# Kernel optimization log

Measured on AMD Instinct MI355X. Metric: run time of the kernel, lower is better.

## Reference

```python
import jax, jax.numpy as jnp
import numpy as np

INPUT_DIM = 32
HIDDEN = 64
BATCH = 4096
SEQ = 256


def _uniform(key, shape, bound):
    return jax.random.uniform(key, shape, dtype=jnp.float32, minval=-bound, maxval=bound)


def setup_inputs() -> dict:
    key = jax.random.key(0)
    ks = jax.random.split(key, 16)
    kb = 1.0 / np.sqrt(HIDDEN)  # torch LSTM/Linear init bound
    x = jax.random.normal(ks[0], (BATCH, SEQ, INPUT_DIM), dtype=jnp.float32)
    # LSTM layer 0 (input_dim -> hidden), gate order i,f,g,o stacked on dim 0
    Wih0 = _uniform(ks[1], (4 * HIDDEN, INPUT_DIM), kb)
    Whh0 = _uniform(ks[2], (4 * HIDDEN, HIDDEN), kb)
    bih0 = _uniform(ks[3], (4 * HIDDEN,), kb)
    bhh0 = _uniform(ks[4], (4 * HIDDEN,), kb)
    # LSTM layer 1 (hidden -> hidden)
    Wih1 = _uniform(ks[5], (4 * HIDDEN, HIDDEN), kb)
    Whh1 = _uniform(ks[6], (4 * HIDDEN, HIDDEN), kb)
    bih1 = _uniform(ks[7], (4 * HIDDEN,), kb)
    bhh1 = _uniform(ks[8], (4 * HIDDEN,), kb)
    # MLP head
    W1 = _uniform(ks[9], (HIDDEN, HIDDEN), kb)
    b1 = _uniform(ks[10], (HIDDEN,), kb)
    W2 = _uniform(ks[11], (1, HIDDEN), kb)
    b2 = _uniform(ks[12], (1,), kb)
    return {"x": x, "Wih0": Wih0, "Whh0": Whh0, "bih0": bih0, "bhh0": bhh0,
            "Wih1": Wih1, "Whh1": Whh1, "bih1": bih1, "bhh1": bhh1,
            "W1": W1, "b1": b1, "W2": W2, "b2": b2}


def lstm_layer(x, Wih, Whh, bih, bhh):
    """x: [B,T,D] -> hidden sequence [B,T,H]. PyTorch gate order i,f,g,o."""
    B = x.shape[0]
    H = Whh.shape[1]
    # precompute input contribution for all timesteps: [B,T,4H]
    gx = jnp.einsum('btd,gd->btg', x, Wih) + bih + bhh

    def step(carry, g_t):
        h, c = carry
        g = g_t + h @ Whh.T  # [B,4H]
        i, f, gg, o = jnp.split(g, 4, axis=-1)
        i = jax.nn.sigmoid(i)
        f = jax.nn.sigmoid(f)
        gg = jnp.tanh(gg)
        o = jax.nn.sigmoid(o)
        c = f * c + i * gg
        h = o * jnp.tanh(c)
        return (h, c), h

    h0 = jnp.zeros((B, H), x.dtype)
    c0 = jnp.zeros((B, H), x.dtype)
    _, hs = jax.lax.scan(step, (h0, c0), jnp.swapaxes(gx, 0, 1))  # hs: [T,B,H]
    return jnp.swapaxes(hs, 0, 1)


def reference(x, Wih0, Whh0, bih0, bhh0, Wih1, Whh1, bih1, bhh1, W1, b1, W2, b2):
    h1 = lstm_layer(x, Wih0, Whh0, bih0, bhh0)    # [B,T,H]
    h2 = lstm_layer(h1, Wih1, Whh1, bih1, bhh1)   # [B,T,H]
    last = h2[:, -1, :]                            # [B,H]
    f = jax.nn.relu(last @ W1.T + b1)              # dropout = identity (eval)
    out = f @ W2.T + b2                            # [B,1]
    return out
```

## Files before the change

### kernel.cpp

```cpp
#include <hip/hip_runtime.h>
#include <cstdint>

typedef __attribute__((ext_vector_type(8))) _Float16 f16x8;
typedef __attribute__((ext_vector_type(4))) float f32x4;

#define SEQL 256

#define WS_B0H   0
#define WS_B0L   49152
#define WS_B1H   98304
#define WS_BIAS0 229376
#define WS_BIAS1 230400

#define ASTR 656
#define L_A  0
#define L_HD 10496
#define HDSTR 272
#define LDS_TOTAL 14848

#define NEG_L   -1.4426950408889634f
#define NEG_2L  -2.8853900817779268f
#define LO_SCALE 2048.0f
#define LO_INV   4.8828125e-4f

__device__ __forceinline__ float ex2(float x) { return __builtin_amdgcn_exp2f(x); }
__device__ __forceinline__ float rcp_(float x) { return __builtin_amdgcn_rcpf(x); }
__device__ __forceinline__ f32x4 mfma16(f16x8 a, f16x8 b, f32x4 c) {
  return __builtin_amdgcn_mfma_f32_16x16x32_f16(a, b, c, 0, 0, 0);
}
__device__ __forceinline__ f16x8 zero8() {
  f16x8 z;
#pragma unroll
  for (int i = 0; i < 8; ++i) z[i] = (_Float16)0.f;
  return z;
}

__global__ __launch_bounds__(256) void prep(
    const float* __restrict__ Wih0, const float* __restrict__ Whh0,
    const float* __restrict__ bih0, const float* __restrict__ bhh0,
    const float* __restrict__ Wih1, const float* __restrict__ Whh1,
    const float* __restrict__ bih1, const float* __restrict__ bhh1,
    unsigned char* __restrict__ ws) {
  int e = blockIdx.x * 256 + threadIdx.x;
  if (e < 24576) {
    int j = e & 7, lane = (e >> 3) & 63, nt = (e >> 9) & 15, ks = e >> 13;
    int kdim = ks * 32 + (lane >> 4) * 8 + j;
    int col = nt * 16 + (lane & 15);
    int ko = col >> 2, g = col & 3;
    float w = (kdim < 32) ? Wih0[(g * 64 + ko) * 32 + kdim]
                          : Whh0[(g * 64 + ko) * 64 + (kdim - 32)];
    w *= (g == 2) ? NEG_2L : NEG_L;
    _Float16 hi = (_Float16)w;
    _Float16 lo = (_Float16)((w - (float)hi) * LO_SCALE);
    ((_Float16*)(ws + WS_B0H))[e] = hi;
    ((_Float16*)(ws + WS_B0L))[e] = lo;
  } else if (e < 57344) {
    int r = e - 24576;
    int j = r & 7, lane = (r >> 3) & 63, nt = (r >> 9) & 15, ks = r >> 13;
    int kdim = ks * 32 + (lane >> 4) * 8 + j;
    int col = nt * 16 + (lane & 15);
    int ko = col >> 2, g = col & 3;
    float w = (kdim < 64) ? Wih1[(g * 64 + ko) * 64 + kdim]
                          : Whh1[(g * 64 + ko) * 64 + (kdim - 64)];
    w *= (g == 2) ? NEG_2L : NEG_L;
    _Float16 hi = (_Float16)w;
    _Float16 lo = (_Float16)((w - (float)hi) * LO_SCALE);
    ((_Float16*)(ws + WS_B1H))[r] = hi;
    ((_Float16*)(ws + WS_B1H + 65536))[r] = lo;
  } else if (e < 57856) {
    int r = e - 57344;
    int col = r & 255, ko = col >> 2, g = col & 3;
    float v = (r < 256) ? bih0[g * 64 + ko] + bhh0[g * 64 + ko]
                        : bih1[g * 64 + ko] + bhh1[g * 64 + ko];
    v *= (g == 2) ? NEG_2L : NEG_L;
    ((float*)(ws + (r < 256 ? WS_BIAS0 : WS_BIAS1)))[col] = v;
  }
}

__global__ __launch_bounds__(1024, 4) void lstm_mfma6(
    const float* __restrict__ x, const unsigned char* __restrict__ ws,
    const float* __restrict__ W1, const float* __restrict__ b1,
    const float* __restrict__ W2, const float* __restrict__ b2,
    float* __restrict__ out) {
  __shared__ __align__(16) unsigned char lds[LDS_TOTAL];
  const int tid = threadIdx.x;
  const int lane = tid & 63, wave = tid >> 6;
  const int q = lane >> 4, bcol = lane & 15;

  f16x8 b0h[3], b0l[3], b1h[4], b1l[4];
#pragma unroll
  for (int ks = 0; ks < 3; ++ks) {
    int rec = (ks * 16 + wave) * 64 + lane;
    b0h[ks] = ((const f16x8*)(ws + WS_B0H))[rec];
    b0l[ks] = ((const f16x8*)(ws + WS_B0L))[rec];
  }
#pragma unroll
  for (int ks = 0; ks < 4; ++ks) {
    int rec = (ks * 16 + wave) * 64 + lane;
    b1h[ks] = ((const f16x8*)(ws + WS_B1H))[rec];
    b1l[ks] = ((const f16x8*)(ws + WS_B1H + 65536))[rec];
  }
  const f32x4 bias0v = ((const f32x4*)(ws + WS_BIAS0))[wave * 4 + q];
  const f32x4 bias1v = ((const f32x4*)(ws + WS_BIAS1))[wave * 4 + q];
  f32x4 z4;
  z4[0] = z4[1] = z4[2] = z4[3] = 0.f;

  for (int i = tid; i < 2624; i += 1024) ((unsigned*)(lds + L_A))[i] = 0u;

  const bool do_x = tid < 512;
  const int bx = tid >> 5, d = tid & 31;
  const float* xcol = x + (size_t)(blockIdx.x * 16 + (do_x ? bx : 0)) * (SEQL * 32) + d;
  if (do_x) {
    *(_Float16*)(lds + L_A + bx * ASTR + d * 2) = (_Float16)xcol[0];
  }

  const int ard = bcol * ASTR + q * 16;
  const int hwr = bcol * ASTR + (wave * 4 + q) * 2;

  float c1 = 0.f, c2 = 0.f, h2f = 0.f;
  f16x8 ah1[2], ah2[2], ax;
  ah1[0] = ah1[1] = ah2[0] = ah2[1] = zero8();
  __syncthreads();
  ax = *(const f16x8*)(lds + L_A + ard + 0);

  auto cell = [&](const f32x4& aH, const f32x4& aL, float& c) -> float {
    float p0 = fmaf(aL[0], LO_INV, aH[0]);
    float p1 = fmaf(aL[1], LO_INV, aH[1]);
    float p2 = fmaf(aL[2], LO_INV, aH[2]);
    float p3 = fmaf(aL[3], LO_INV, aH[3]);
    float gi = rcp_(1.f + ex2(p0));
    float gf = rcp_(1.f + ex2(p1));
    float gg = fmaf(2.f, rcp_(1.f + ex2(p2)), -1.f);
    float go = rcp_(1.f + ex2(p3));
    c = fmaf(gf, c, gi * gg);
    float tc = fmaf(2.f, rcp_(1.f + ex2(c * NEG_2L)), -1.f);
    return go * tc;
  };

  auto iter = [&](int t, int par, bool doL2) {
    const int h1s = 128 + par * 128;
    const int h2s = 384 + par * 128;
    const int xwr = (par ^ 1) * 64;
    float xnext = 0.f;
    if (do_x && t < SEQL - 1) xnext = xcol[(t + 1) * 32];

    f32x4 aH0 = mfma16(b0h[0], ax, bias0v);
    f32x4 aL0 = mfma16(b0l[0], ax, z4);
    f32x4 aH1 = mfma16(b1h[0], ah1[0], bias1v);
    f32x4 aL1 = mfma16(b1l[0], ah1[0], z4);
    aH1 = mfma16(b1h[1], ah1[1], aH1);
    aL1 = mfma16(b1l[1], ah1[1], aL1);
#pragma unroll
    for (int ks = 0; ks < 2; ++ks) {
      aH0 = mfma16(b0h[ks + 1], ah1[ks], aH0);
      aL0 = mfma16(b0l[ks + 1], ah1[ks], aL0);
      aH1 = mfma16(b1h[ks + 2], ah2[ks], aH1);
      aL1 = mfma16(b1l[ks + 2], ah2[ks], aL1);
    }
    float h1 = cell(aH0, aL0, c1);
    *(_Float16*)(lds + L_A + hwr + h1s) = (_Float16)h1;
    if (doL2) {
      float h2 = cell(aH1, aL1, c2);
      *(_Float16*)(lds + L_A + hwr + h2s) = (_Float16)h2;
    }
    if (do_x && t < SEQL - 1) {
      *(_Float16*)(lds + L_A + bx * ASTR + xwr + d * 2) = (_Float16)xnext;
    }
    __syncthreads();
    ah1[0] = *(const f16x8*)(lds + L_A + ard + h1s);
    ah1[1] = *(const f16x8*)(lds + L_A + ard + h1s + 64);
    ah2[0] = *(const f16x8*)(lds + L_A + ard + h2s);
    ah2[1] = *(const f16x8*)(lds + L_A + ard + h2s + 64);
    ax     = *(const f16x8*)(lds + L_A + ard + xwr);
  };

  iter(0, 0, false);
#pragma unroll 1
  for (int tp = 0; tp < 127; ++tp) {
    iter(2 * tp + 1, 1, true);
    iter(2 * tp + 2, 0, true);
  }
  iter(255, 1, true);

  {
    f32x4 aH = mfma16(b1h[0], ah1[0], bias1v);
    f32x4 aL = mfma16(b1l[0], ah1[0], z4);
    aH = mfma16(b1h[1], ah1[1], aH);
    aL = mfma16(b1l[1], ah1[1], aL);
#pragma unroll
    for (int ks = 0; ks < 2; ++ks) {
      aH = mfma16(b1h[ks + 2], ah2[ks], aH);
      aL = mfma16(b1l[ks + 2], ah2[ks], aL);
    }
    h2f = cell(aH, aL, c2);
  }

  __syncthreads();
  *(float*)(lds + L_HD + bcol * HDSTR + (wave * 4 + q) * 4) = h2f;
  __syncthreads();
  if (tid < 256) {
    const int s = tid & 15, bo = tid >> 4;
    const float* h2row = (const float*)(lds + L_HD + bo * HDSTR);
    float partial = 0.f;
#pragma unroll
    for (int kk4 = 0; kk4 < 4; ++kk4) {
      int kk = s * 4 + kk4;
      float f = b1[kk];
#pragma unroll
      for (int j = 0; j < 64; j += 4) {
        f32x4 w = *(const f32x4*)(W1 + kk * 64 + j);
        f = fmaf(w[0], h2row[j], f);
        f = fmaf(w[1], h2row[j + 1], f);
        f = fmaf(w[2], h2row[j + 2], f);
        f = fmaf(w[3], h2row[j + 3], f);
      }
      f = fmaxf(f, 0.f);
      partial = fmaf(f, W2[kk], partial);
    }
    partial += __shfl_xor(partial, 8, 64);
    partial += __shfl_xor(partial, 4, 64);
    partial += __shfl_xor(partial, 2, 64);
    partial += __shfl_xor(partial, 1, 64);
    if (s == 0) out[blockIdx.x * 16 + bo] = partial + b2[0];
  }
}

extern "C" void kernel_launch(void* const* d_in, const int* in_sizes, int n_in,
                              void* d_out, int out_size, void* d_ws, size_t ws_size,
                              hipStream_t stream) {
  const float* x    = (const float*)d_in[0];
  const float* Wih0 = (const float*)d_in[1];
  const float* Whh0 = (const float*)d_in[2];
  const float* bih0 = (const float*)d_in[3];
  const float* bhh0 = (const float*)d_in[4];
  const float* Wih1 = (const float*)d_in[5];
  const float* Whh1 = (const float*)d_in[6];
  const float* bih1 = (const float*)d_in[7];
  const float* bhh1 = (const float*)d_in[8];
  const float* W1   = (const float*)d_in[9];
  const float* b1   = (const float*)d_in[10];
  const float* W2   = (const float*)d_in[11];
  const float* b2   = (const float*)d_in[12];
  unsigned char* ws = (unsigned char*)d_ws;
  float* out = (float*)d_out;

  prep<<<(57856 + 255) / 256, 256, 0, stream>>>(Wih0, Whh0, bih0, bhh0,
                                                Wih1, Whh1, bih1, bhh1, ws);
  lstm_mfma6<<<256, 1024, 0, stream>>>(x, ws, W1, b1, W2, b2, out);
}
```

Baseline: 442.9 us.

## Specialize waves per LSTM layer and load x directly into registers

Splits the 16 waves into two groups: 8 waves compute layer 0 and 8 compute layer 1, with each wave owning two column tiles. Before, every wave computed a slice of both layers. The input x is now read straight from global memory into MFMA operand registers with one step of prefetch, replacing the LDS staging path, and the LDS layout shrinks to match. This cuts redundant operand reads and x staging per step, but doubles the MFMA chain length per wave and may leave the two wave groups unevenly loaded.

After: 541.6 us. 1.22x slower.

```diff
diff --git a/kernel.cpp b/kernel.cpp
--- a/kernel.cpp
+++ b/kernel.cpp
@@ -12,11 +12,11 @@
 #define WS_BIAS0 229376
 #define WS_BIAS1 230400
 
-#define ASTR 656
+#define ASTR 528
 #define L_A  0
-#define L_HD 10496
+#define L_HD 8448
 #define HDSTR 272
-#define LDS_TOTAL 14848
+#define LDS_TOTAL 12800
 
 #define NEG_L   -1.4426950408889634f
 #define NEG_2L  -2.8853900817779268f
@@ -28,11 +28,13 @@
 __device__ __forceinline__ f32x4 mfma16(f16x8 a, f16x8 b, f32x4 c) {
   return __builtin_amdgcn_mfma_f32_16x16x32_f16(a, b, c, 0, 0, 0);
 }
-__device__ __forceinline__ f16x8 zero8() {
-  f16x8 z;
-#pragma unroll
-  for (int i = 0; i < 8; ++i) z[i] = (_Float16)0.f;
-  return z;
+__device__ __forceinline__ f16x8 cvt8(f32x4 a, f32x4 b) {
+  f16x8 r;
+#pragma unroll
+  for (int j = 0; j < 4; ++j) r[j] = (_Float16)a[j];
+#pragma unroll
+  for (int j = 0; j < 4; ++j) r[4 + j] = (_Float16)b[j];
+  return r;
 }
 
 __global__ __launch_bounds__(256) void prep(
@@ -77,7 +79,7 @@
   }
 }
 
-__global__ __launch_bounds__(1024, 4) void lstm_mfma6(
+__global__ __launch_bounds__(1024, 4) void lstm_mfma7(
     const float* __restrict__ x, const unsigned char* __restrict__ ws,
     const float* __restrict__ W1, const float* __restrict__ b1,
     const float* __restrict__ W2, const float* __restrict__ b2,
@@ -86,42 +88,49 @@
   const int tid = threadIdx.x;
   const int lane = tid & 63, wave = tid >> 6;
   const int q = lane >> 4, bcol = lane & 15;
-
-  f16x8 b0h[3], b0l[3], b1h[4], b1l[4];
-#pragma unroll
-  for (int ks = 0; ks < 3; ++ks) {
-    int rec = (ks * 16 + wave) * 64 + lane;
-    b0h[ks] = ((const f16x8*)(ws + WS_B0H))[rec];
-    b0l[ks] = ((const f16x8*)(ws + WS_B0L))[rec];
-  }
-#pragma unroll
-  for (int ks = 0; ks < 4; ++ks) {
-    int rec = (ks * 16 + wave) * 64 + lane;
-    b1h[ks] = ((const f16x8*)(ws + WS_B1H))[rec];
-    b1l[ks] = ((const f16x8*)(ws + WS_B1H + 65536))[rec];
-  }
-  const f32x4 bias0v = ((const f32x4*)(ws + WS_BIAS0))[wave * 4 + q];
-  const f32x4 bias1v = ((const f32x4*)(ws + WS_BIAS1))[wave * 4 + q];
+  const int wtype = wave >> 3;
+  const int wn = wave & 7;
+
+  f16x8 wh[2][4], wl[2][4];
+  if (wtype == 0) {
+#pragma unroll
+    for (int m = 0; m < 2; ++m)
+#pragma unroll
+      for (int ks = 0; ks < 3; ++ks) {
+        int rec = (ks * 16 + (wn + 8 * m)) * 64 + lane;
+        wh[m][ks] = ((const f16x8*)(ws + WS_B0H))[rec];
+        wl[m][ks] = ((const f16x8*)(ws + WS_B0L))[rec];
+      }
+  } else {
+#pragma unroll
+    for (int m = 0; m < 2; ++m)
+#pragma unroll
+      for (int ks = 0; ks < 4; ++ks) {
+        int rec = (ks * 16 + (wn + 8 * m)) * 64 + lane;
+        wh[m][ks] = ((const f16x8*)(ws + WS_B1H))[rec];
+        wl[m][ks] = ((const f16x8*)(ws + WS_B1H + 65536))[rec];
+      }
+  }
+  const f32x4* bp = (const f32x4*)(ws + (wtype ? WS_BIAS1 : WS_BIAS0));
+  const f32x4 bias0v = bp[4 * wn + q];
+  const f32x4 bias1v = bp[4 * (wn + 8) + q];
   f32x4 z4;
   z4[0] = z4[1] = z4[2] = z4[3] = 0.f;
 
-  for (int i = tid; i < 2624; i += 1024) ((unsigned*)(lds + L_A))[i] = 0u;
-
-  const bool do_x = tid < 512;
-  const int bx = tid >> 5, d = tid & 31;
-  const float* xcol = x + (size_t)(blockIdx.x * 16 + (do_x ? bx : 0)) * (SEQL * 32) + d;
-  if (do_x) {
-    *(_Float16*)(lds + L_A + bx * ASTR + d * 2) = (_Float16)xcol[0];
-  }
-
-  const int ard = bcol * ASTR + q * 16;
-  const int hwr = bcol * ASTR + (wave * 4 + q) * 2;
-
-  float c1 = 0.f, c2 = 0.f, h2f = 0.f;
-  f16x8 ah1[2], ah2[2], ax;
-  ah1[0] = ah1[1] = ah2[0] = ah2[1] = zero8();
+  for (int i2 = tid; i2 < 2112; i2 += 1024) ((unsigned*)lds)[i2] = 0u;
+
+  const float* xp = x + (size_t)(blockIdx.x * 16 + bcol) * (SEQL * 32) + q * 8;
+  f16x8 ax;
+  f32x4 xna, xnb;
+  if (wtype == 0) {
+    f32x4 a0 = *(const f32x4*)(xp);
+    f32x4 b0v = *(const f32x4*)(xp + 4);
+    ax = cvt8(a0, b0v);
+    xna = *(const f32x4*)(xp + 32);
+    xnb = *(const f32x4*)(xp + 36);
+  }
+  float cc0 = 0.f, cc1 = 0.f;
   __syncthreads();
-  ax = *(const f16x8*)(lds + L_A + ard + 0);
 
   auto cell = [&](const f32x4& aH, const f32x4& aL, float& c) -> float {
     float p0 = fmaf(aL[0], LO_INV, aH[0]);
@@ -137,41 +146,60 @@
     return go * tc;
   };
 
-  auto iter = [&](int t, int par, bool doL2) {
-    const int h1s = 128 + par * 128;
-    const int h2s = 384 + par * 128;
-    const int xwr = (par ^ 1) * 64;
-    float xnext = 0.f;
-    if (do_x && t < SEQL - 1) xnext = xcol[(t + 1) * 32];
-
-    f32x4 aH0 = mfma16(b0h[0], ax, bias0v);
-    f32x4 aL0 = mfma16(b0l[0], ax, z4);
-    f32x4 aH1 = mfma16(b1h[0], ah1[0], bias1v);
-    f32x4 aL1 = mfma16(b1l[0], ah1[0], z4);
-    aH1 = mfma16(b1h[1], ah1[1], aH1);
-    aL1 = mfma16(b1l[1], ah1[1], aL1);
-#pragma unroll
-    for (int ks = 0; ks < 2; ++ks) {
-      aH0 = mfma16(b0h[ks + 1], ah1[ks], aH0);
-      aL0 = mfma16(b0l[ks + 1], ah1[ks], aL0);
-      aH1 = mfma16(b1h[ks + 2], ah2[ks], aH1);
-      aL1 = mfma16(b1l[ks + 2], ah2[ks], aL1);
-    }
-    float h1 = cell(aH0, aL0, c1);
-    *(_Float16*)(lds + L_A + hwr + h1s) = (_Float16)h1;
-    if (doL2) {
-      float h2 = cell(aH1, aL1, c2);
-      *(_Float16*)(lds + L_A + hwr + h2s) = (_Float16)h2;
-    }
-    if (do_x && t < SEQL - 1) {
-      *(_Float16*)(lds + L_A + bx * ASTR + xwr + d * 2) = (_Float16)xnext;
+  auto iter = [&](int i, int par, bool doL2) {
+    const int rb = bcol * ASTR;
+    f16x8 ah1a = *(const f16x8*)(lds + rb + (par ^ 1) * 128 + q * 16);
+    f16x8 ah1b = *(const f16x8*)(lds + rb + (par ^ 1) * 128 + 64 + q * 16);
+    if (wtype == 0) {
+      f32x4 aH0 = mfma16(wh[0][0], ax, bias0v);
+      f32x4 aL0 = mfma16(wl[0][0], ax, z4);
+      f32x4 aH1 = mfma16(wh[1][0], ax, bias1v);
+      f32x4 aL1 = mfma16(wl[1][0], ax, z4);
+      aH0 = mfma16(wh[0][1], ah1a, aH0);
+      aL0 = mfma16(wl[0][1], ah1a, aL0);
+      aH1 = mfma16(wh[1][1], ah1a, aH1);
+      aL1 = mfma16(wl[1][1], ah1a, aL1);
+      aH0 = mfma16(wh[0][2], ah1b, aH0);
+      aL0 = mfma16(wl[0][2], ah1b, aL0);
+      aH1 = mfma16(wh[1][2], ah1b, aH1);
+      aL1 = mfma16(wl[1][2], ah1b, aL1);
+      float h0 = cell(aH0, aL0, cc0);
+      float h1v = cell(aH1, aL1, cc1);
+      const int wb = rb + par * 128;
+      *(_Float16*)(lds + wb + (4 * wn + q) * 2) = (_Float16)h0;
+      *(_Float16*)(lds + wb + (4 * (wn + 8) + q) * 2) = (_Float16)h1v;
+      ax = cvt8(xna, xnb);
+      int tn = i + 2; if (tn > SEQL - 1) tn = SEQL - 1;
+      xna = *(const f32x4*)(xp + tn * 32);
+      xnb = *(const f32x4*)(xp + tn * 32 + 4);
+    } else {
+      f16x8 ah2a = *(const f16x8*)(lds + rb + 256 + par * 128 + q * 16);
+      f16x8 ah2b = *(const f16x8*)(lds + rb + 256 + par * 128 + 64 + q * 16);
+      f32x4 aH0 = mfma16(wh[0][0], ah1a, bias0v);
+      f32x4 aL0 = mfma16(wl[0][0], ah1a, z4);
+      f32x4 aH1 = mfma16(wh[1][0], ah1a, bias1v);
+      f32x4 aL1 = mfma16(wl[1][0], ah1a, z4);
+      aH0 = mfma16(wh[0][1], ah1b, aH0);
+      aL0 = mfma16(wl[0][1], ah1b, aL0);
+      aH1 = mfma16(wh[1][1], ah1b, aH1);
+      aL1 = mfma16(wl[1][1], ah1b, aL1);
+      aH0 = mfma16(wh[0][2], ah2a, aH0);
+      aL0 = mfma16(wl[0][2], ah2a, aL0);
+      aH1 = mfma16(wh[1][2], ah2a, aH1);
+      aL1 = mfma16(wl[1][2], ah2a, aL1);
+      aH0 = mfma16(wh[0][3], ah2b, aH0);
+      aL0 = mfma16(wl[0][3], ah2b, aL0);
+      aH1 = mfma16(wh[1][3], ah2b, aH1);
+      aL1 = mfma16(wl[1][3], ah2b, aL1);
+      if (doL2) {
+        float h0 = cell(aH0, aL0, cc0);
+        float h1v = cell(aH1, aL1, cc1);
+        const int wb = rb + 256 + (par ^ 1) * 128;
+        *(_Float16*)(lds + wb + (4 * wn + q) * 2) = (_Float16)h0;
+        *(_Float16*)(lds + wb + (4 * (wn + 8) + q) * 2) = (_Float16)h1v;
+      }
     }
     __syncthreads();
-    ah1[0] = *(const f16x8*)(lds + L_A + ard + h1s);
-    ah1[1] = *(const f16x8*)(lds + L_A + ard + h1s + 64);
-    ah2[0] = *(const f16x8*)(lds + L_A + ard + h2s);
-    ah2[1] = *(const f16x8*)(lds + L_A + ard + h2s + 64);
-    ax     = *(const f16x8*)(lds + L_A + ard + xwr);
   };
 
   iter(0, 0, false);
@@ -182,22 +210,35 @@
   }
   iter(255, 1, true);
 
-  {
-    f32x4 aH = mfma16(b1h[0], ah1[0], bias1v);
-    f32x4 aL = mfma16(b1l[0], ah1[0], z4);
-    aH = mfma16(b1h[1], ah1[1], aH);
-    aL = mfma16(b1l[1], ah1[1], aL);
-#pragma unroll
-    for (int ks = 0; ks < 2; ++ks) {
-      aH = mfma16(b1h[ks + 2], ah2[ks], aH);
-      aL = mfma16(b1l[ks + 2], ah2[ks], aL);
-    }
-    h2f = cell(aH, aL, c2);
-  }
-
+  if (wtype == 1) {
+    const int rb = bcol * ASTR;
+    f16x8 a1 = *(const f16x8*)(lds + rb + 128 + q * 16);
+    f16x8 a1b = *(const f16x8*)(lds + rb + 128 + 64 + q * 16);
+    f16x8 a2 = *(const f16x8*)(lds + rb + 256 + q * 16);
+    f16x8 a2b = *(const f16x8*)(lds + rb + 256 + 64 + q * 16);
+    f32x4 aH0 = mfma16(wh[0][0], a1, bias0v);
+    f32x4 aL0 = mfma16(wl[0][0], a1, z4);
+    f32x4 aH1 = mfma16(wh[1][0], a1, bias1v);
+    f32x4 aL1 = mfma16(wl[1][0], a1, z4);
+    aH0 = mfma16(wh[0][1], a1b, aH0);
+    aL0 = mfma16(wl[0][1], a1b, aL0);
+    aH1 = mfma16(wh[1][1], a1b, aH1);
+    aL1 = mfma16(wl[1][1], a1b, aL1);
+    aH0 = mfma16(wh[0][2], a2, aH0);
+    aL0 = mfma16(wl[0][2], a2, aL0);
+    aH1 = mfma16(wh[1][2], a2, aH1);
+    aL1 = mfma16(wl[1][2], a2, aL1);
+    aH0 = mfma16(wh[0][3], a2b, aH0);
+    aL0 = mfma16(wl[0][3], a2b, aL0);
+    aH1 = mfma16(wh[1][3], a2b, aH1);
+    aL1 = mfma16(wl[1][3], a2b, aL1);
+    float h2f0 = cell(aH0, aL0, cc0);
+    float h2f1 = cell(aH1, aL1, cc1);
+    *(float*)(lds + L_HD + bcol * HDSTR + (4 * wn + q) * 4) = h2f0;
+    *(float*)(lds + L_HD + bcol * HDSTR + (4 * (wn + 8) + q) * 4) = h2f1;
+  }
   __syncthreads();
-  *(float*)(lds + L_HD + bcol * HDSTR + (wave * 4 + q) * 4) = h2f;
-  __syncthreads();
+
   if (tid < 256) {
     const int s = tid & 15, bo = tid >> 4;
     const float* h2row = (const float*)(lds + L_HD + bo * HDSTR);
@@ -246,5 +287,5 @@
 
   prep<<<(57856 + 255) / 256, 256, 0, stream>>>(Wih0, Whh0, bih0, bhh0,
                                                 Wih1, Whh1, bih1, bhh1, ws);
-  lstm_mfma6<<<256, 1024, 0, stream>>>(x, ws, W1, b1, W2, b2, out);
-}
+  lstm_mfma7<<<256, 1024, 0, stream>>>(x, ws, W1, b1, W2, b2, out);
+}
```

## Halve block to 8 waves, each computing two gate tiles, load x directly to registers

Applied to the files above, without the earlier changes.

The LSTM kernel now uses 512 threads (8 waves) per 16-sequence block instead of 1024, and each wave computes two 16-column gate tiles, doubling its register-held weights and MFMA work per step. The input x is read straight from global memory into the MFMA operand registers two steps ahead, which removes the LDS x staging buffer and shrinks the LDS row stride. The aim is to cut the per-timestep barrier cost and LDS traffic by syncing fewer waves and giving each wave more independent MFMAs to interleave. In exchange, register pressure is higher and each wave carries a longer serial chain of work per step.

Measured after the change: 460.2 us. 1.04x slower.

```diff
diff --git a/kernel.cpp b/kernel.cpp
--- a/kernel.cpp
+++ b/kernel.cpp
@@ -12,11 +12,10 @@
 #define WS_BIAS0 229376
 #define WS_BIAS1 230400
 
-#define ASTR 656
-#define L_A  0
-#define L_HD 10496
+#define ASTR 528
+#define L_HD 8448
 #define HDSTR 272
-#define LDS_TOTAL 14848
+#define LDS_TOTAL 12800
 
 #define NEG_L   -1.4426950408889634f
 #define NEG_2L  -2.8853900817779268f
@@ -33,6 +32,14 @@
 #pragma unroll
   for (int i = 0; i < 8; ++i) z[i] = (_Float16)0.f;
   return z;
+}
+__device__ __forceinline__ f16x8 cvt8(f32x4 a, f32x4 b) {
+  f16x8 r;
+#pragma unroll
+  for (int j = 0; j < 4; ++j) r[j] = (_Float16)a[j];
+#pragma unroll
+  for (int j = 0; j < 4; ++j) r[4 + j] = (_Float16)b[j];
+  return r;
 }
 
 __global__ __launch_bounds__(256) void prep(
@@ -77,7 +84,7 @@
   }
 }
 
-__global__ __launch_bounds__(1024, 4) void lstm_mfma6(
+__global__ __launch_bounds__(512, 2) void lstm_mfma9(
     const float* __restrict__ x, const unsigned char* __restrict__ ws,
     const float* __restrict__ W1, const float* __restrict__ b1,
     const float* __restrict__ W2, const float* __restrict__ b2,
@@ -85,43 +92,51 @@
   __shared__ __align__(16) unsigned char lds[LDS_TOTAL];
   const int tid = threadIdx.x;
   const int lane = tid & 63, wave = tid >> 6;
-  const int q = lane >> 4, bcol = lane & 15;
-
-  f16x8 b0h[3], b0l[3], b1h[4], b1l[4];
-#pragma unroll
-  for (int ks = 0; ks < 3; ++ks) {
-    int rec = (ks * 16 + wave) * 64 + lane;
-    b0h[ks] = ((const f16x8*)(ws + WS_B0H))[rec];
-    b0l[ks] = ((const f16x8*)(ws + WS_B0L))[rec];
-  }
-#pragma unroll
-  for (int ks = 0; ks < 4; ++ks) {
-    int rec = (ks * 16 + wave) * 64 + lane;
-    b1h[ks] = ((const f16x8*)(ws + WS_B1H))[rec];
-    b1l[ks] = ((const f16x8*)(ws + WS_B1H + 65536))[rec];
-  }
-  const f32x4 bias0v = ((const f32x4*)(ws + WS_BIAS0))[wave * 4 + q];
-  const f32x4 bias1v = ((const f32x4*)(ws + WS_BIAS1))[wave * 4 + q];
+  const int q = lane >> 4, mcol = lane & 15;
+
+  f16x8 w0h[2][3], w0l[2][3], w1h[2][4], w1l[2][4];
+#pragma unroll
+  for (int m = 0; m < 2; ++m) {
+    const int nt = wave + 8 * m;
+#pragma unroll
+    for (int ks = 0; ks < 3; ++ks) {
+      int rec = (ks * 16 + nt) * 64 + lane;
+      w0h[m][ks] = ((const f16x8*)(ws + WS_B0H))[rec];
+      w0l[m][ks] = ((const f16x8*)(ws + WS_B0L))[rec];
+    }
+#pragma unroll
+    for (int ks = 0; ks < 4; ++ks) {
+      int rec = (ks * 16 + nt) * 64 + lane;
+      w1h[m][ks] = ((const f16x8*)(ws + WS_B1H))[rec];
+      w1l[m][ks] = ((const f16x8*)(ws + WS_B1H + 65536))[rec];
+    }
+  }
+  f32x4 b0v[2], b1v[2];
+#pragma unroll
+  for (int m = 0; m < 2; ++m) {
+    b0v[m] = ((const f32x4*)(ws + WS_BIAS0))[4 * (wave + 8 * m) + q];
+    b1v[m] = ((const f32x4*)(ws + WS_BIAS1))[4 * (wave + 8 * m) + q];
+  }
   f32x4 z4;
   z4[0] = z4[1] = z4[2] = z4[3] = 0.f;
 
-  for (int i = tid; i < 2624; i += 1024) ((unsigned*)(lds + L_A))[i] = 0u;
-
-  const bool do_x = tid < 512;
-  const int bx = tid >> 5, d = tid & 31;
-  const float* xcol = x + (size_t)(blockIdx.x * 16 + (do_x ? bx : 0)) * (SEQL * 32) + d;
-  if (do_x) {
-    *(_Float16*)(lds + L_A + bx * ASTR + d * 2) = (_Float16)xcol[0];
-  }
-
-  const int ard = bcol * ASTR + q * 16;
-  const int hwr = bcol * ASTR + (wave * 4 + q) * 2;
-
-  float c1 = 0.f, c2 = 0.f, h2f = 0.f;
-  f16x8 ah1[2], ah2[2], ax;
+  for (int i = tid; i < 2112; i += 512) ((unsigned*)lds)[i] = 0u;
+
+  const float* xp = x + (size_t)(blockIdx.x * 16 + mcol) * (SEQL * 32) + q * 8;
+  f32x4 x0a = *(const f32x4*)(xp);
+  f32x4 x0b = *(const f32x4*)(xp + 4);
+  f16x8 ax = cvt8(x0a, x0b);
+  f32x4 xna = *(const f32x4*)(xp + 32);
+  f32x4 xnb = *(const f32x4*)(xp + 36);
+
+  const int ard = mcol * ASTR + q * 16;
+  const int wr0 = mcol * ASTR + (4 * wave + q) * 2;
+  const int wr1 = mcol * ASTR + (4 * wave + 32 + q) * 2;
+
+  float c1[2] = {0.f, 0.f}, c2[2] = {0.f, 0.f};
+  f16x8 ah1[2], ah2[2];
   ah1[0] = ah1[1] = ah2[0] = ah2[1] = zero8();
   __syncthreads();
-  ax = *(const f16x8*)(lds + L_A + ard + 0);
 
   auto cell = [&](const f32x4& aH, const f32x4& aL, float& c) -> float {
     float p0 = fmaf(aL[0], LO_INV, aH[0]);
@@ -138,40 +153,56 @@
   };
 
   auto iter = [&](int t, int par, bool doL2) {
-    const int h1s = 128 + par * 128;
-    const int h2s = 384 + par * 128;
-    const int xwr = (par ^ 1) * 64;
-    float xnext = 0.f;
-    if (do_x && t < SEQL - 1) xnext = xcol[(t + 1) * 32];
-
-    f32x4 aH0 = mfma16(b0h[0], ax, bias0v);
-    f32x4 aL0 = mfma16(b0l[0], ax, z4);
-    f32x4 aH1 = mfma16(b1h[0], ah1[0], bias1v);
-    f32x4 aL1 = mfma16(b1l[0], ah1[0], z4);
-    aH1 = mfma16(b1h[1], ah1[1], aH1);
-    aL1 = mfma16(b1l[1], ah1[1], aL1);
-#pragma unroll
-    for (int ks = 0; ks < 2; ++ks) {
-      aH0 = mfma16(b0h[ks + 1], ah1[ks], aH0);
-      aL0 = mfma16(b0l[ks + 1], ah1[ks], aL0);
-      aH1 = mfma16(b1h[ks + 2], ah2[ks], aH1);
-      aL1 = mfma16(b1l[ks + 2], ah2[ks], aL1);
-    }
-    float h1 = cell(aH0, aL0, c1);
-    *(_Float16*)(lds + L_A + hwr + h1s) = (_Float16)h1;
+    const int h1s = par * 128;
+    const int h2s = 256 + par * 128;
+    f32x4 aH0[2], aL0[2], aH1[2], aL1[2];
+    aH0[0] = mfma16(w0h[0][0], ax, b0v[0]);
+    aH0[1] = mfma16(w0h[1][0], ax, b0v[1]);
+    aL0[0] = mfma16(w0l[0][0], ax, z4);
+    aL0[1] = mfma16(w0l[1][0], ax, z4);
+    aH1[0] = mfma16(w1h[0][0], ah1[0], b1v[0]);
+    aH1[1] = mfma16(w1h[1][0], ah1[0], b1v[1]);
+    aL1[0] = mfma16(w1l[0][0], ah1[0], z4);
+    aL1[1] = mfma16(w1l[1][0], ah1[0], z4);
+    aH0[0] = mfma16(w0h[0][1], ah1[0], aH0[0]);
+    aH0[1] = mfma16(w0h[1][1], ah1[0], aH0[1]);
+    aL0[0] = mfma16(w0l[0][1], ah1[0], aL0[0]);
+    aL0[1] = mfma16(w0l[1][1], ah1[0], aL0[1]);
+    aH0[0] = mfma16(w0h[0][2], ah1[1], aH0[0]);
+    aH0[1] = mfma16(w0h[1][2], ah1[1], aH0[1]);
+    aL0[0] = mfma16(w0l[0][2], ah1[1], aL0[0]);
+    aL0[1] = mfma16(w0l[1][2], ah1[1], aL0[1]);
+    aH1[0] = mfma16(w1h[0][1], ah1[1], aH1[0]);
+    aH1[1] = mfma16(w1h[1][1], ah1[1], aH1[1]);
+    aL1[0] = mfma16(w1l[0][1], ah1[1], aL1[0]);
+    aL1[1] = mfma16(w1l[1][1], ah1[1], aL1[1]);
+    aH1[0] = mfma16(w1h[0][2], ah2[0], aH1[0]);
+    aH1[1] = mfma16(w1h[1][2], ah2[0], aH1[1]);
+    aL1[0] = mfma16(w1l[0][2], ah2[0], aL1[0]);
+    aL1[1] = mfma16(w1l[1][2], ah2[0], aL1[1]);
+    aH1[0] = mfma16(w1h[0][3], ah2[1], aH1[0]);
+    aH1[1] = mfma16(w1h[1][3], ah2[1], aH1[1]);
+    aL1[0] = mfma16(w1l[0][3], ah2[1], aL1[0]);
+    aL1[1] = mfma16(w1l[1][3], ah2[1], aL1[1]);
+    float h10 = cell(aH0[0], aL0[0], c1[0]);
+    float h11 = cell(aH0[1], aL0[1], c1[1]);
+    *(_Float16*)(lds + wr0 + h1s) = (_Float16)h10;
+    *(_Float16*)(lds + wr1 + h1s) = (_Float16)h11;
     if (doL2) {
-      float h2 = cell(aH1, aL1, c2);
-      *(_Float16*)(lds + L_A + hwr + h2s) = (_Float16)h2;
-    }
-    if (do_x && t < SEQL - 1) {
-      *(_Float16*)(lds + L_A + bx * ASTR + xwr + d * 2) = (_Float16)xnext;
-    }
+      float h20 = cell(aH1[0], aL1[0], c2[0]);
+      float h21 = cell(aH1[1], aL1[1], c2[1]);
+      *(_Float16*)(lds + wr0 + h2s) = (_Float16)h20;
+      *(_Float16*)(lds + wr1 + h2s) = (_Float16)h21;
+    }
+    ax = cvt8(xna, xnb);
+    int tn = t + 2; if (tn > SEQL - 1) tn = SEQL - 1;
+    xna = *(const f32x4*)(xp + tn * 32);
+    xnb = *(const f32x4*)(xp + tn * 32 + 4);
     __syncthreads();
-    ah1[0] = *(const f16x8*)(lds + L_A + ard + h1s);
-    ah1[1] = *(const f16x8*)(lds + L_A + ard + h1s + 64);
-    ah2[0] = *(const f16x8*)(lds + L_A + ard + h2s);
-    ah2[1] = *(const f16x8*)(lds + L_A + ard + h2s + 64);
-    ax     = *(const f16x8*)(lds + L_A + ard + xwr);
+    ah1[0] = *(const f16x8*)(lds + ard + h1s);
+    ah1[1] = *(const f16x8*)(lds + ard + h1s + 64);
+    ah2[0] = *(const f16x8*)(lds + ard + h2s);
+    ah2[1] = *(const f16x8*)(lds + ard + h2s + 64);
   };
 
   iter(0, 0, false);
@@ -183,21 +214,30 @@
   iter(255, 1, true);
 
   {
-    f32x4 aH = mfma16(b1h[0], ah1[0], bias1v);
-    f32x4 aL = mfma16(b1l[0], ah1[0], z4);
-    aH = mfma16(b1h[1], ah1[1], aH);
-    aL = mfma16(b1l[1], ah1[1], aL);
-#pragma unroll
-    for (int ks = 0; ks < 2; ++ks) {
-      aH = mfma16(b1h[ks + 2], ah2[ks], aH);
-      aL = mfma16(b1l[ks + 2], ah2[ks], aL);
-    }
-    h2f = cell(aH, aL, c2);
-  }
-
+    f32x4 aH[2], aL[2];
+    aH[0] = mfma16(w1h[0][0], ah1[0], b1v[0]);
+    aH[1] = mfma16(w1h[1][0], ah1[0], b1v[1]);
+    aL[0] = mfma16(w1l[0][0], ah1[0], z4);
+    aL[1] = mfma16(w1l[1][0], ah1[0], z4);
+    aH[0] = mfma16(w1h[0][1], ah1[1], aH[0]);
+    aH[1] = mfma16(w1h[1][1], ah1[1], aH[1]);
+    aL[0] = mfma16(w1l[0][1], ah1[1], aL[0]);
+    aL[1] = mfma16(w1l[1][1], ah1[1], aL[1]);
+    aH[0] = mfma16(w1h[0][2], ah2[0], aH[0]);
+    aH[1] = mfma16(w1h[1][2], ah2[0], aH[1]);
+    aL[0] = mfma16(w1l[0][2], ah2[0], aL[0]);
+    aL[1] = mfma16(w1l[1][2], ah2[0], aL[1]);
+    aH[0] = mfma16(w1h[0][3], ah2[1], aH[0]);
+    aH[1] = mfma16(w1h[1][3], ah2[1], aH[1]);
+    aL[0] = mfma16(w1l[0][3], ah2[1], aL[0]);
+    aL[1] = mfma16(w1l[1][3], ah2[1], aL[1]);
+    float h20 = cell(aH[0], aL[0], c2[0]);
+    float h21 = cell(aH[1], aL[1], c2[1]);
+    *(float*)(lds + L_HD + mcol * HDSTR + (4 * wave + q) * 4) = h20;
+    *(float*)(lds + L_HD + mcol * HDSTR + (4 * wave + 32 + q) * 4) = h21;
+  }
   __syncthreads();
-  *(float*)(lds + L_HD + bcol * HDSTR + (wave * 4 + q) * 4) = h2f;
-  __syncthreads();
+
   if (tid < 256) {
     const int s = tid & 15, bo = tid >> 4;
     const float* h2row = (const float*)(lds + L_HD + bo * HDSTR);
@@ -246,5 +286,5 @@
 
   prep<<<(57856 + 255) / 256, 256, 0, stream>>>(Wih0, Whh0, bih0, bhh0,
                                                 Wih1, Whh1, bih1, bhh1, ws);
-  lstm_mfma6<<<256, 1024, 0, stream>>>(x, ws, W1, b1, W2, b2, out);
-}
+  lstm_mfma9<<<256, 512, 0, stream>>>(x, ws, W1, b1, W2, b2, out);
+}
```
